# Performance work log

Measured on AMD Instinct MI355X. Metric: run time of the kernel, lower is better.

Reference implementation:

```python
import jax, jax.numpy as jnp
import numpy as np

B, H, S = 16, 1024, 2048

def setup_inputs() -> dict:
    key = jax.random.key(0)
    kf, kz, ki = jax.random.split(key, 3)
    f = jax.random.uniform(kf, (B, H, S), dtype=jnp.float32)
    z = jax.random.normal(kz, (B, H, S), dtype=jnp.float32)
    i = jax.random.uniform(ki, (B, H, S), dtype=jnp.float32)
    return {"f": f, "z": z, "i": i}

def reference(f, z, i):
    # Inputs are [batch, hidden, seq]; recurrence runs over seq:
    #   h_t = f_t * h_{t-1} + i_t * z_t, h_{-1} = 0
    fs = jnp.transpose(f, (2, 0, 1))  # [S, B, H]
    xs = jnp.transpose(i * z, (2, 0, 1))  # [S, B, H]

    def step(h_prev, fx):
        f_t, x_t = fx
        h_t = f_t * h_prev + x_t
        return h_t, h_t

    h0 = jnp.zeros(fs.shape[1:], dtype=fs.dtype)
    _, hs = jax.lax.scan(step, h0, (fs, xs))  # [S, B, H]
    return jnp.transpose(hs, (1, 2, 0))  # [B, H, S]
```

## Files before the change

kernel.cpp:

```cpp
#include <hip/hip_runtime.h>


constexpr int S_LEN = 2048;
constexpr int TPB   = 512;

__global__ __launch_bounds__(TPB) void ifo_scan_kernel(
    const float* __restrict__ f,
    const float* __restrict__ z,
    const float* __restrict__ iin,
    float* __restrict__ out)
{
    const size_t base = (size_t)blockIdx.x * S_LEN;
    const int t    = threadIdx.x;
    const int lane = t & 63;
    const int wave = t >> 6;

    const float4 ff = reinterpret_cast<const float4*>(f   + base)[t];
    const float4 zz = reinterpret_cast<const float4*>(z   + base)[t];
    const float4 ii = reinterpret_cast<const float4*>(iin + base)[t];

    float4 xx;
    xx.x = ii.x * zz.x;
    xx.y = ii.y * zz.y;
    xx.z = ii.z * zz.z;
    xx.w = ii.w * zz.w;

    float A = ff.x, B = xx.x;
    A = ff.y * A;  B = ff.y * B + xx.y;
    A = ff.z * A;  B = ff.z * B + xx.z;
    A = ff.w * A;  B = ff.w * B + xx.w;

    float a = A, b = B;
    #pragma unroll
    for (int d = 1; d < 64; d <<= 1) {
        float a_up = __shfl_up(a, d);
        float b_up = __shfl_up(b, d);
        if (lane >= d) {
            b = a * b_up + b;
            a = a * a_up;
        }
    }

    __shared__ float wa[8], wb[8];
    if (lane == 63) { wa[wave] = a; wb[wave] = b; }
    __syncthreads();

    float pa = 1.0f, pb = 0.0f;
    for (int w = 0; w < wave; ++w) {
        pb = wa[w] * pb + wb[w];
        pa = wa[w] * pa;
    }

    float ea = __shfl_up(a, 1);
    float eb = __shfl_up(b, 1);
    if (lane == 0) { ea = 1.0f; eb = 0.0f; }

    float h = ea * pb + eb;
    (void)pa;

    float4 oo;
    h = ff.x * h + xx.x;  oo.x = h;
    h = ff.y * h + xx.y;  oo.y = h;
    h = ff.z * h + xx.z;  oo.z = h;
    h = ff.w * h + xx.w;  oo.w = h;
    reinterpret_cast<float4*>(out + base)[t] = oo;
}

extern "C" void kernel_launch(void* const* d_in, const int* in_sizes, int n_in,
                              void* d_out, int out_size, void* d_ws, size_t ws_size,
                              hipStream_t stream) {
    const float* f = (const float*)d_in[0];
    const float* z = (const float*)d_in[1];
    const float* i = (const float*)d_in[2];
    float* out = (float*)d_out;

    const int rows = out_size / S_LEN;
    ifo_scan_kernel<<<rows, TPB, 0, stream>>>(f, z, i, out);
}
```

Baseline: 381.1 us.

## Scan each row within a single wave in four passes with register prefetch

```diff
diff --git a/kernel.cpp b/kernel.cpp
--- a/kernel.cpp
+++ b/kernel.cpp
@@ -1,69 +1,100 @@
 #include <hip/hip_runtime.h>
 
 
-constexpr int S_LEN = 2048;
-constexpr int TPB   = 512;
+constexpr int S_LEN  = 2048;
+constexpr int WAVES  = 4;
+constexpr int TPB    = 64 * WAVES;
+constexpr int PASSES = 4;
+constexpr int PASS_E = S_LEN / PASSES;
 
-__global__ __launch_bounds__(TPB) void ifo_scan_kernel(
+__global__ __launch_bounds__(TPB, 8) void ifo_scan_wave(
     const float* __restrict__ f,
     const float* __restrict__ z,
     const float* __restrict__ iin,
     float* __restrict__ out)
 {
-    const size_t base = (size_t)blockIdx.x * S_LEN;
-    const int t    = threadIdx.x;
-    const int lane = t & 63;
-    const int wave = t >> 6;
+    const int lane = threadIdx.x & 63;
+    const int wv   = threadIdx.x >> 6;
+    const size_t row  = (size_t)blockIdx.x * WAVES + wv;
+    const size_t base = row * S_LEN;
 
-    const float4 ff = reinterpret_cast<const float4*>(f   + base)[t];
-    const float4 zz = reinterpret_cast<const float4*>(z   + base)[t];
-    const float4 ii = reinterpret_cast<const float4*>(iin + base)[t];
+    const float4* F = reinterpret_cast<const float4*>(f   + base);
+    const float4* Z = reinterpret_cast<const float4*>(z   + base);
+    const float4* I = reinterpret_cast<const float4*>(iin + base);
+    float4*       O = reinterpret_cast<float4*>(out + base);
 
-    float4 xx;
-    xx.x = ii.x * zz.x;
-    xx.y = ii.y * zz.y;
-    xx.z = ii.z * zz.z;
-    xx.w = ii.w * zz.w;
+    const int c0 = lane * 2;
+    const int c1 = lane * 2 + 1;
+    const int pstride = PASS_E / 4;
 
-    float A = ff.x, B = xx.x;
-    A = ff.y * A;  B = ff.y * B + xx.y;
-    A = ff.z * A;  B = ff.z * B + xx.z;
-    A = ff.w * A;  B = ff.w * B + xx.w;
+    float4 f0 = F[c0], f1 = F[c1];
+    float4 z0 = Z[c0], z1 = Z[c1];
+    float4 i0 = I[c0], i1 = I[c1];
 
-    float a = A, b = B;
+    float H = 0.0f;
+
     #pragma unroll
-    for (int d = 1; d < 64; d <<= 1) {
-        float a_up = __shfl_up(a, d);
-        float b_up = __shfl_up(b, d);
-        if (lane >= d) {
-            b = a * b_up + b;
-            a = a * a_up;
+    for (int p = 0; p < PASSES; ++p) {
+        float4 nf0, nf1, nz0, nz1, ni0, ni1;
+        if (p + 1 < PASSES) {
+            const int o = (p + 1) * pstride;
+            nf0 = F[o + c0]; nf1 = F[o + c1];
+            nz0 = Z[o + c0]; nz1 = Z[o + c1];
+            ni0 = I[o + c0]; ni1 = I[o + c1];
         }
+
+        float4 x0, x1;
+        x0.x = i0.x * z0.x; x0.y = i0.y * z0.y;
+        x0.z = i0.z * z0.z; x0.w = i0.w * z0.w;
+        x1.x = i1.x * z1.x; x1.y = i1.y * z1.y;
+        x1.z = i1.z * z1.z; x1.w = i1.w * z1.w;
+
+        float a = f0.x, b = x0.x;
+        a = f0.y * a;  b = f0.y * b + x0.y;
+        a = f0.z * a;  b = f0.z * b + x0.z;
+        a = f0.w * a;  b = f0.w * b + x0.w;
+        a = f1.x * a;  b = f1.x * b + x1.x;
+        a = f1.y * a;  b = f1.y * b + x1.y;
+        a = f1.z * a;  b = f1.z * b + x1.z;
+        a = f1.w * a;  b = f1.w * b + x1.w;
+
+        #pragma unroll
+        for (int d = 1; d < 64; d <<= 1) {
+            float a_up = __shfl_up(a, d);
+            float b_up = __shfl_up(b, d);
+            if (lane >= d) {
+                b = a * b_up + b;
+                a = a * a_up;
+            }
+        }
+
+        float ea = __shfl_up(a, 1);
+        float eb = __shfl_up(b, 1);
+        if (lane == 0) { ea = 1.0f; eb = 0.0f; }
+        float h = ea * H + eb;
+
+        float4 o0, o1;
+        h = f0.x * h + x0.x;  o0.x = h;
+        h = f0.y * h + x0.y;  o0.y = h;
+        h = f0.z * h + x0.z;  o0.z = h;
+        h = f0.w * h + x0.w;  o0.w = h;
+        h = f1.x * h + x1.x;  o1.x = h;
+        h = f1.y * h + x1.y;  o1.y = h;
+        h = f1.z * h + x1.z;  o1.z = h;
+        h = f1.w * h + x1.w;  o1.w = h;
+
+        const int o = p * pstride;
+        O[o + c0] = o0;
+        O[o + c1] = o1;
+
+        float A63 = __shfl(a, 63);
+        float B63 = __shfl(b, 63);
+        H = A63 * H + B63;
+
+        f0 = nf0; f1 = nf1;
+        z0 = nz0; z1 = nz1;
+        i0 = ni0; i1 = ni1;
     }
-
-    __shared__ float wa[8], wb[8];
-    if (lane == 63) { wa[wave] = a; wb[wave] = b; }
-    __syncthreads();
-
-    float pa = 1.0f, pb = 0.0f;
-    for (int w = 0; w < wave; ++w) {
-        pb = wa[w] * pb + wb[w];
-        pa = wa[w] * pa;
-    }
-
-    float ea = __shfl_up(a, 1);
-    float eb = __shfl_up(b, 1);
-    if (lane == 0) { ea = 1.0f; eb = 0.0f; }
-
-    float h = ea * pb + eb;
-    (void)pa;
-
-    float4 oo;
-    h = ff.x * h + xx.x;  oo.x = h;
-    h = ff.y * h + xx.y;  oo.y = h;
-    h = ff.z * h + xx.z;  oo.z = h;
-    h = ff.w * h + xx.w;  oo.w = h;
-    reinterpret_cast<float4*>(out + base)[t] = oo;
 }
 
 extern "C" void kernel_launch(void* const* d_in, const int* in_sizes, int n_in,
@@ -75,5 +106,5 @@
     float* out = (float*)d_out;
 
     const int rows = out_size / S_LEN;
-    ifo_scan_kernel<<<rows, TPB, 0, stream>>>(f, z, i, out);
+    ifo_scan_wave<<<rows / WAVES, TPB, 0, stream>>>(f, z, i, out);
 }
```

Result: slower. 391.8 us (+2.8%).
